# Optimization experiments

Measured on AMD Instinct MI355X. Metric: run time of the kernel, lower is better.

The kernel has to match this reference:

```python
import jax, jax.numpy as jnp
import numpy as np

H = 512
W = 512
N_STROKES = 5000
S = 10          # samples_per_curve
K = 20          # strokes_per_pixel
CANVAS_COLOR = 0.5  # 'gray'
COARSE = 5      # coarse grid downsample factor (H//5, W//5)


def setup_inputs() -> dict:
    key = jax.random.key(0)
    ks = jax.random.split(key, 6)
    # stroke centers spread over the canvas
    location = jax.random.uniform(ks[0], (N_STROKES, 2), jnp.float32) * jnp.array([H, W], jnp.float32)
    # bezier control-point offsets relative to the stroke center
    curve_s = jax.random.normal(ks[1], (N_STROKES, 2), jnp.float32) * 8.0
    curve_e = jax.random.normal(ks[2], (N_STROKES, 2), jnp.float32) * 8.0
    curve_c = jax.random.normal(ks[3], (N_STROKES, 2), jnp.float32) * 8.0
    color = jax.random.uniform(ks[4], (N_STROKES, 3), jnp.float32)
    width = jax.random.uniform(ks[5], (N_STROKES, 1), jnp.float32) * 4.0 + 1.0
    return {"curve_s": curve_s, "curve_e": curve_e, "curve_c": curve_c,
            "color": color, "location": location, "width": width}


def _bezier_points(s, c, e, num_points):
    # s, c, e: [N, 2] -> [N, num_points, 2]
    t = jnp.linspace(0.0, 1.0, num_points).astype(jnp.float32)  # [S]
    omt2 = (1.0 - t) ** 2  # [S]
    t2 = t ** 2
    # x/y computed identically: c + (1-t)^2 (s - c) + t^2 (e - c)
    pts = c[:, None, :] + omt2[None, :, None] * (s - c)[:, None, :] \
          + t2[None, :, None] * (e - c)[:, None, :]
    return pts  # [N, S, 2]


def _nearest_upsample_idx(out_size, in_size):
    # torch F.interpolate mode='nearest': src = floor(dst * in/out)
    idx = jnp.floor(jnp.arange(out_size) * (in_size / out_size)).astype(jnp.int32)
    return jnp.clip(idx, 0, in_size - 1)


def reference(curve_s, curve_e, curve_c, color, location, width):
    # sample bezier curve points (absolute coords)
    pts = _bezier_points(curve_s + location, curve_c + location,
                         curve_e + location, S)  # [N, S, 2]

    # ---- coarse-grid KNN over stroke centers ----
    Hc, Wc = H // COARSE, W // COARSE
    tH = jnp.linspace(0.0, float(H), Hc).astype(jnp.float32)
    tW = jnp.linspace(0.0, float(W), Wc).astype(jnp.float32)
    Px, Py = jnp.meshgrid(tH, tW, indexing='ij')
    P = jnp.stack([Px, Py], axis=-1)  # [Hc, Wc, 2]
    D_centers = jnp.sum(jnp.square(P[:, :, None, :] - location), axis=-1)  # [Hc, Wc, N]
    _, idcs = jax.lax.top_k(-D_centers, K)  # [Hc, Wc, K]

    near_pts = pts[idcs]      # [Hc, Wc, K, S, 2]
    near_col = color[idcs]    # [Hc, Wc, K, 3]
    near_w = width[idcs]      # [Hc, Wc, K, 1]

    # ---- upsample coarse gathers to full res ----
    ih = _nearest_upsample_idx(H, Hc)
    iw = _nearest_upsample_idx(W, Wc)
    near_pts = near_pts[ih][:, iw]   # [H, W, K, S, 2] (nearest)
    near_col = near_col[ih][:, iw]   # [H, W, K, 3]   (nearest)
    # widths: bilinear (align_corners=False, no antialias) per channel
    near_w = jax.image.resize(near_w[..., 0], (H, W, K), method='linear')[..., None]  # [H, W, K, 1]

    # ---- full-res pixel grid ----
    tHf = jnp.linspace(0.0, float(H), H).astype(jnp.float32)
    tWf = jnp.linspace(0.0, float(W), W).astype(jnp.float32)
    Pxf, Pyf = jnp.meshgrid(tHf, tWf, indexing='ij')
    P_full = jnp.stack([Pxf, Pyf], axis=-1)  # [H, W, 2]

    # ---- per-pixel closest point on each polyline segment ----
    a = near_pts[:, :, :, :S - 1, :]              # [H, W, K, S-1, 2]
    b_a = near_pts[:, :, :, 1:, :] - a            # segment direction
    pa = P_full[:, :, None, None, :] - a          # pixel - segment start
    t = jnp.sum(b_a * pa, axis=-1) / jnp.sum(jnp.square(b_a), axis=-1)
    t = jnp.clip(t, 0.0, 1.0)
    closest = a + t[..., None] * b_a
    dist = jnp.sum(jnp.square(P_full[:, :, None, None, :] - closest), axis=-1)  # [H, W, K, S-1]

    D = jnp.min(dist, axis=(-1, -2))  # [H, W]
    min_per_stroke = jnp.min(dist, axis=-1)  # [H, W, K]
    ranking = jax.nn.softmax(100000.0 * (1.0 / (1e-08 + min_per_stroke)), axis=-1)  # [H, W, K]

    I_colors = jnp.einsum('hwkf,hwk->hwf', near_col, ranking)  # [H, W, 3]
    bs = jnp.einsum('hwkf,hwk->hwf', near_w, ranking)          # [H, W, 1]
    bs_mask = jax.nn.sigmoid(bs - D[..., None])
    canvas = jnp.full_like(I_colors, CANVAS_COLOR)
    I = I_colors * bs_mask + (1.0 - bs_mask) * canvas
    return I
```

## Files before the change

kernel.cpp:

```cpp
#include <hip/hip_runtime.h>
#include <math.h>

#define NS 5000
#define SS 10
#define KK 20
#define HC 102
#define NBIN 32
#define BINW 16.0f
#define NPB 20
#define CAP 192

#define WAVE_SYNC() __asm__ volatile("s_waitcnt lgkmcnt(0)" ::: "memory")

__global__ void __launch_bounds__(256) prep_kernel(
        const float* __restrict__ cs, const float* __restrict__ ce,
        const float* __restrict__ cc, const float* __restrict__ loc,
        const float* __restrict__ color, const float* __restrict__ width,
        float* __restrict__ sdata, float4* __restrict__ ctab,
        int* __restrict__ binCntP) {
    __shared__ int4 lcnt4[NBIN*NBIN/4];
    int* lcnt = (int*)lcnt4;
    int t = threadIdx.x;
    lcnt4[t] = make_int4(0, 0, 0, 0);
    __syncthreads();
    int i = blockIdx.x * 256 + t;
    if (i < NS) {
        float lx = loc[i*2+0], ly = loc[i*2+1];
        float sx = cs[i*2+0] + lx, sy = cs[i*2+1] + ly;
        float ex = ce[i*2+0] + lx, ey = ce[i*2+1] + ly;
        float px = cc[i*2+0] + lx, py = cc[i*2+1] + ly;
        float qx[SS], qy[SS];
        #pragma unroll
        for (int j = 0; j < SS; ++j) {
            float tt = (float)j * (1.0f / 9.0f);
            float omt = 1.0f - tt;
            float omt2 = omt * omt, t2 = tt * tt;
            qx[j] = px + omt2 * (sx - px) + t2 * (ex - px);
            qy[j] = py + omt2 * (sy - py) + t2 * (ey - py);
            sdata[i*32 + 2*j + 0] = qx[j];
            sdata[i*32 + 2*j + 1] = qy[j];
        }
        #pragma unroll
        for (int sg = 0; sg < 9; ++sg) {
            float bx = qx[sg+1] - qx[sg], by = qy[sg+1] - qy[sg];
            sdata[i*32 + 20 + sg] = 1.0f / (bx*bx + by*by);
        }
        sdata[i*32 + 29] = 0.0f; sdata[i*32 + 30] = 0.0f; sdata[i*32 + 31] = 0.0f;
        ctab[i] = make_float4(color[i*3+0], color[i*3+1], color[i*3+2], width[i]);
        int b0 = min(max((int)(lx * (1.0f/BINW)), 0), NBIN-1);
        int b1 = min(max((int)(ly * (1.0f/BINW)), 0), NBIN-1);
        atomicAdd(&lcnt[b0*NBIN + b1], 1);
    }
    __syncthreads();
    ((int4*)binCntP)[blockIdx.x * 256 + t] = lcnt4[t];
}

__global__ void __launch_bounds__(256) scatter_kernel(
        const float* __restrict__ loc, const int* __restrict__ binCntP,
        int* __restrict__ binStart, float2* __restrict__ sxy, int* __restrict__ sid) {
    __shared__ int fill[NBIN*NBIN];
    __shared__ int wsum[4];
    int t = threadIdx.x, lane = t & 63, w = t >> 6;
    int mb = blockIdx.x;
    int4 tot = make_int4(0,0,0,0), bel = make_int4(0,0,0,0);
    for (int b = 0; b < NPB; ++b) {
        int4 v = ((const int4*)binCntP)[b * 256 + t];
        tot.x += v.x; tot.y += v.y; tot.z += v.z; tot.w += v.w;
        if (b < mb) { bel.x += v.x; bel.y += v.y; bel.z += v.z; bel.w += v.w; }
    }
    int s0 = tot.x, s1 = s0 + tot.y, s2 = s1 + tot.z, s3 = s2 + tot.w;
    int x = s3;
    #pragma unroll
    for (int off = 1; off < 64; off <<= 1) {
        int y = __shfl_up(x, off, 64);
        if (lane >= off) x += y;
    }
    if (lane == 63) wsum[w] = x;
    __syncthreads();
    int woff = 0;
    #pragma unroll
    for (int i = 0; i < 4; ++i) woff += (i < w) ? wsum[i] : 0;
    int texcl = woff + x - s3;
    fill[4*t+0] = texcl      + bel.x;
    fill[4*t+1] = texcl + s0 + bel.y;
    fill[4*t+2] = texcl + s1 + bel.z;
    fill[4*t+3] = texcl + s2 + bel.w;
    if (mb == 0) {
        binStart[4*t+1] = texcl + s0;
        binStart[4*t+2] = texcl + s1;
        binStart[4*t+3] = texcl + s2;
        binStart[4*t+4] = texcl + s3;
        if (t == 0) binStart[0] = 0;
    }
    __syncthreads();
    int i = mb * 256 + t;
    if (i < NS) {
        float l0 = loc[i*2+0], l1 = loc[i*2+1];
        int b0 = min(max((int)(l0 * (1.0f/BINW)), 0), NBIN-1);
        int b1 = min(max((int)(l1 * (1.0f/BINW)), 0), NBIN-1);
        int pos = atomicAdd(&fill[b0*NBIN + b1], 1);
        sxy[pos] = make_float2(l0, l1);
        sid[pos] = i;
    }
}

__global__ void __launch_bounds__(256) topk_kernel(const float* __restrict__ loc,
                                                   const float* __restrict__ width,
                                                   const float2* __restrict__ sxy,
                                                   const int* __restrict__ sid,
                                                   const int* __restrict__ binStart,
                                                   int* __restrict__ idcs,
                                                   float* __restrict__ wk) {
    __shared__ unsigned long long sk[4][CAP];
    int w = threadIdx.x >> 6, lane = threadIdx.x & 63;
    int cell = blockIdx.x * 4 + w;
    int ci = cell / HC, cj = cell - ci * HC;
    const float dc = 512.0f / 101.0f;
    float c0 = (float)ci * dc;
    float c1 = (float)cj * dc;
    unsigned long long below = (1ull << lane) - 1ull;

    float R = 26.0f;
    int cnt = 0;
    for (int attempt = 0; attempt < 5; ++attempt) {
        float R2 = R * R;
        int base = 0;
        int by0 = max((int)((c0 - R) * (1.0f/BINW)), 0);
        int by1 = min((int)((c0 + R) * (1.0f/BINW)), NBIN-1);
        int bx0 = max((int)((c1 - R) * (1.0f/BINW)), 0);
        int bx1 = min((int)((c1 + R) * (1.0f/BINW)), NBIN-1);
        int nrows = by1 - by0 + 1;
        if (nrows <= 6) {
            int rs[6], re[6];
            #pragma unroll
            for (int r = 0; r < 6; ++r) {
                bool va = (r < nrows);
                int by = va ? (by0 + r) : by0;
                rs[r] = binStart[by*NBIN + bx0];
                re[r] = va ? binStart[by*NBIN + bx1 + 1] : rs[r];
            }
            float2 pr[6]; int idr[6];
            #pragma unroll
            for (int r = 0; r < 6; ++r) {
                int t  = rs[r] + lane;
                int tc = max(min(t, re[r] - 1), 0);
                pr[r]  = sxy[tc];
                idr[r] = sid[tc];
            }
            #pragma unroll
            for (int r = 0; r < 6; ++r) {
                int t = rs[r] + lane;
                float dx = c0 - pr[r].x, dy = c1 - pr[r].y;
                float d = dx*dx + dy*dy;
                bool pred = (t < re[r]) && (d < R2);
                unsigned long long mask = __ballot(pred);
                int pos = base + __popcll(mask & below);
                if (pred && pos < CAP)
                    sk[w][pos] = ((unsigned long long)__float_as_uint(d) << 32)
                               | (unsigned int)idr[r];
                base += __popcll(mask);
                for (int t0 = rs[r] + 64; t0 < re[r]; t0 += 64) {
                    int t2  = t0 + lane;
                    int tc2 = min(t2, re[r] - 1);
                    float2 p = sxy[tc2];
                    float ex = c0 - p.x, ey = c1 - p.y;
                    float d2 = ex*ex + ey*ey;
                    bool p2 = (t2 < re[r]) && (d2 < R2);
                    unsigned long long m2 = __ballot(p2);
                    int pos2 = base + __popcll(m2 & below);
                    if (p2 && pos2 < CAP)
                        sk[w][pos2] = ((unsigned long long)__float_as_uint(d2) << 32)
                                    | (unsigned int)sid[tc2];
                    base += __popcll(m2);
                }
            }
        } else {
            for (int by = by0; by <= by1; ++by) {
                int s = binStart[by*NBIN + bx0];
                int e = binStart[by*NBIN + bx1 + 1];
                for (int t0 = s; t0 < e; t0 += 64) {
                    int t = t0 + lane;
                    int tc = min(t, e - 1);
                    float2 p = sxy[tc];
                    float dx = c0 - p.x, dy = c1 - p.y;
                    float d = dx*dx + dy*dy;
                    bool pred = (t < e) && (d < R2);
                    unsigned long long mask = __ballot(pred);
                    int pos = base + __popcll(mask & below);
                    if (pred && pos < CAP)
                        sk[w][pos] = ((unsigned long long)__float_as_uint(d) << 32)
                                   | (unsigned int)sid[tc];
                    base += __popcll(mask);
                }
            }
        }
        cnt = base;
        if (cnt >= KK) break;
        R *= 1.6f;
    }
    WAVE_SYNC();

    if (cnt >= KK && cnt <= CAP) {
        if (cnt <= 64) {
            unsigned long long k0 = (lane < cnt) ? sk[w][lane] : ~0ull;
            int r0 = 0;
            int j = 0;
            #pragma unroll 1
            for (; j + 4 <= cnt; j += 4) {
                unsigned long long a = sk[w][j],   b = sk[w][j+1];
                unsigned long long c = sk[w][j+2], d = sk[w][j+3];
                r0 += (int)(a < k0) + (int)(b < k0) + (int)(c < k0) + (int)(d < k0);
            }
            for (; j < cnt; ++j) r0 += (int)(sk[w][j] < k0);
            if (r0 < KK && lane < cnt) {
                int idx = (int)(unsigned int)(k0 & 0xffffffffull);
                idcs[cell*KK + r0] = idx;
                wk[cell*KK + r0]   = width[idx];
            }
        } else {
            unsigned long long k0 = (lane       < cnt) ? sk[w][lane]       : ~0ull;
            unsigned long long k1 = (lane + 64  < cnt) ? sk[w][lane + 64]  : ~0ull;
            unsigned long long k2 = (lane + 128 < cnt) ? sk[w][lane + 128] : ~0ull;
            int r0 = 0, r1 = 0, r2 = 0;
            #pragma unroll 1
            for (int j = 0; j < cnt; ++j) {
                unsigned long long a = sk[w][j];
                r0 += (int)(a < k0); r1 += (int)(a < k1); r2 += (int)(a < k2);
            }
            if (r0 < KK && lane < cnt) {
                int idx = (int)(unsigned int)(k0 & 0xffffffffull);
                idcs[cell*KK + r0] = idx;  wk[cell*KK + r0] = width[idx];
            }
            if (r1 < KK && lane + 64 < cnt) {
                int idx = (int)(unsigned int)(k1 & 0xffffffffull);
                idcs[cell*KK + r1] = idx;  wk[cell*KK + r1] = width[idx];
            }
            if (r2 < KK && lane + 128 < cnt) {
                int idx = (int)(unsigned int)(k2 & 0xffffffffull);
                idcs[cell*KK + r2] = idx;  wk[cell*KK + r2] = width[idx];
            }
        }
    } else {
        if (lane == 0) {
            float bd[KK]; int bi[KK];
            for (int k = 0; k < KK; ++k) { bd[k] = 3.4e38f; bi[k] = 0; }
            for (int n = 0; n < NS; ++n) {
                float dx = c0 - loc[n*2+0];
                float dy = c1 - loc[n*2+1];
                float d = dx*dx + dy*dy;
                if (d < bd[KK-1]) {
                    int p = KK - 1;
                    while (p > 0 && bd[p-1] > d) { bd[p] = bd[p-1]; bi[p] = bi[p-1]; --p; }
                    bd[p] = d; bi[p] = n;
                }
            }
            for (int k = 0; k < KK; ++k) {
                idcs[cell*KK + k] = bi[k];
                wk[cell*KK + k]   = width[bi[k]];
            }
        }
    }
}

__global__ void __launch_bounds__(256, 4) render_kernel(const float* __restrict__ sdata,
                                                        const float4* __restrict__ ctab,
                                                        const int* __restrict__ idcs,
                                                        const float* __restrict__ wk,
                                                        float* __restrict__ out) {
    __shared__ float wvl[256][21];
    int tt0 = threadIdx.x, lane = tt0 & 63, wq = tt0 >> 6;
    int x = blockIdx.x * 16 + ((wq & 1) << 3) + (lane & 7);
    int y = blockIdx.y * 16 + ((wq >> 1) << 3) + (lane >> 3);
    const float df = 512.0f / 511.0f;
    float p0 = (float)y * df;
    float p1 = (float)x * df;
    int cy = (y * 51) >> 8;
    int cx = (x * 51) >> 8;

    const int4* mip = (const int4*)(idcs + (cy * HC + cx) * KK);
    int4 m0 = mip[0], m1 = mip[1], m2 = mip[2], m3 = mip[3], m4 = mip[4];
    int idxs[KK] = {m0.x,m0.y,m0.z,m0.w, m1.x,m1.y,m1.z,m1.w, m2.x,m2.y,m2.z,m2.w,
                    m3.x,m3.y,m3.z,m3.w, m4.x,m4.y,m4.z,m4.w};

    const float sc = 102.0f / 512.0f;
    float iny = ((float)y + 0.5f) * sc - 0.5f;
    float inx = ((float)x + 0.5f) * sc - 0.5f;
    float y0f = floorf(iny), x0f = floorf(inx);
    float fy = iny - y0f, fx = inx - x0f;
    int y0 = min(max((int)y0f, 0), HC - 1);
    int y1 = min(max((int)y0f + 1, 0), HC - 1);
    int x0 = min(max((int)x0f, 0), HC - 1);
    int x1 = min(max((int)x0f + 1, 0), HC - 1);
    const float4* q00 = (const float4*)(wk + (y0 * HC + x0) * KK);
    const float4* q01 = (const float4*)(wk + (y0 * HC + x1) * KK);
    const float4* q10 = (const float4*)(wk + (y1 * HC + x0) * KK);
    const float4* q11 = (const float4*)(wk + (y1 * HC + x1) * KK);

    #pragma unroll
    for (int r = 0; r < 5; ++r) {
        float4 a = q00[r], b = q01[r], c = q10[r], d = q11[r];
        wvl[tt0][4*r+0] = (1.0f - fy) * ((1.0f - fx) * a.x + fx * b.x)
                        +          fy * ((1.0f - fx) * c.x + fx * d.x);
        wvl[tt0][4*r+1] = (1.0f - fy) * ((1.0f - fx) * a.y + fx * b.y)
                        +          fy * ((1.0f - fx) * c.y + fx * d.y);
        wvl[tt0][4*r+2] = (1.0f - fy) * ((1.0f - fx) * a.z + fx * b.z)
                        +          fy * ((1.0f - fx) * c.z + fx * d.z);
        wvl[tt0][4*r+3] = (1.0f - fy) * ((1.0f - fx) * a.w + fx * b.w)
                        +          fy * ((1.0f - fx) * c.w + fx * d.w);
    }

    float m = -INFINITY, s = 0.0f;
    float a0 = 0.0f, a1 = 0.0f, a2 = 0.0f, wa = 0.0f;
    float D = INFINITY;

    #pragma unroll 4
    for (int k = 0; k < KK; ++k) {
        const float4* sp = (const float4*)(sdata + idxs[k] * 32);
        float4 f0 = sp[0], f1 = sp[1], f2 = sp[2], f3 = sp[3], f4 = sp[4];
        float4 i0 = sp[5], i1 = sp[6], i2 = sp[7];
        float4 cw = ctab[idxs[k]];
        float qx[10] = {f0.x, f0.z, f1.x, f1.z, f2.x, f2.z, f3.x, f3.z, f4.x, f4.z};
        float qy[10] = {f0.y, f0.w, f1.y, f1.w, f2.y, f2.w, f3.y, f3.w, f4.y, f4.w};
        float iv[9]  = {i0.x, i0.y, i0.z, i0.w, i1.x, i1.y, i1.z, i1.w, i2.x};
        float mink = INFINITY;
        #pragma unroll
        for (int sg = 0; sg < 9; ++sg) {
            float ax = qx[sg], ay = qy[sg];
            float bx = qx[sg+1] - ax, by = qy[sg+1] - ay;
            float pax = p0 - ax, pay = p1 - ay;
            float dot = bx * pax + by * pay;
            float tt = dot * iv[sg];
            tt = fminf(fmaxf(tt, 0.0f), 1.0f);
            float ccx = ax + tt * bx, ccy = ay + tt * by;
            float ddx = p0 - ccx, ddy = p1 - ccy;
            float d = ddx * ddx + ddy * ddy;
            mink = fminf(mink, d);
        }
        D = fminf(D, mink);
        float z = 100000.0f / (1e-8f + mink);
        float nm  = fmaxf(m, z);
        float scl = __expf(m - nm);
        float e   = __expf(z - nm);
        s  = s  * scl + e;
        a0 = a0 * scl + cw.x * e;
        a1 = a1 * scl + cw.y * e;
        a2 = a2 * scl + cw.z * e;
        wa = wa * scl + wvl[tt0][k] * e;
        m = nm;
    }
    float inv = 1.0f / s;
    float bs = wa * inv;
    float msk = 1.0f / (1.0f + __expf(-(bs - D)));
    float o0 = a0 * inv * msk + (1.0f - msk) * 0.5f;
    float o1 = a1 * inv * msk + (1.0f - msk) * 0.5f;
    float o2 = a2 * inv * msk + (1.0f - msk) * 0.5f;
    int base = (y * 512 + x) * 3;
    out[base+0] = o0;
    out[base+1] = o1;
    out[base+2] = o2;
}

extern "C" void kernel_launch(void* const* d_in, const int* in_sizes, int n_in,
                              void* d_out, int out_size, void* d_ws, size_t ws_size,
                              hipStream_t stream) {
    const float* cs    = (const float*)d_in[0];
    const float* ce    = (const float*)d_in[1];
    const float* cc    = (const float*)d_in[2];
    const float* color = (const float*)d_in[3];
    const float* loc   = (const float*)d_in[4];
    const float* width = (const float*)d_in[5];
    float* out = (float*)d_out;

    char* p = (char*)d_ws;
    float*  sdata    = (float*)p;                 p += NS * 32 * sizeof(float);
    float4* ctab     = (float4*)p;                p += NS * sizeof(float4);
    int*    idcs     = (int*)p;                   p += (size_t)HC*HC*KK*sizeof(int);
    float*  wk       = (float*)p;                 p += (size_t)HC*HC*KK*sizeof(float);
    int*    binCntP  = (int*)p;                   p += NPB * NBIN*NBIN * sizeof(int);
    int*    binStart = (int*)p;                   p += 4112;
    float2* sxy      = (float2*)p;                p += NS * sizeof(float2);
    int*    sid      = (int*)p;

    prep_kernel   <<<NPB, 256, 0, stream>>>(cs, ce, cc, loc, color, width, sdata, ctab, binCntP);
    scatter_kernel<<<NPB, 256, 0, stream>>>(loc, binCntP, binStart, sxy, sid);
    topk_kernel   <<<(HC*HC)/4, 256, 0, stream>>>(loc, width, sxy, sid, binStart, idcs, wk);
    render_kernel <<<dim3(32, 32), 256, 0, stream>>>(sdata, ctab, idcs, wk, out);
}
```

Measured before the change: 128.3 us.

## Stage per-block stroke records and colors in LDS for render kernel

The render kernel now loads, for each 16x16 pixel block, the up to 16 coarse cells it covers. It copies their 20 stroke indices, 32-float stroke records and color entries into shared memory once per block. The inner loop then reads them from LDS rather than gathering from global memory per pixel. The bilinear width interpolation moves into the loop and reads global wk directly instead of going through a per-thread LDS array. This cuts redundant scattered global loads but uses about 47 KB of LDS per block, which may lower occupancy below the launch-bounds target, and it adds a staging phase with two barriers.

```diff
diff --git a/kernel.cpp b/kernel.cpp
--- a/kernel.cpp
+++ b/kernel.cpp
@@ -267,20 +267,34 @@
                                                         const int* __restrict__ idcs,
                                                         const float* __restrict__ wk,
                                                         float* __restrict__ out) {
-    __shared__ float wvl[256][21];
+    __shared__ float  srec[16*20*32];
+    __shared__ float4 scol[16*20];
+    __shared__ int    sidx[16*20];
     int tt0 = threadIdx.x, lane = tt0 & 63, wq = tt0 >> 6;
     int x = blockIdx.x * 16 + ((wq & 1) << 3) + (lane & 7);
     int y = blockIdx.y * 16 + ((wq >> 1) << 3) + (lane >> 3);
+    int cy0 = (blockIdx.y * 16 * 51) >> 8;
+    int cx0 = (blockIdx.x * 16 * 51) >> 8;
+
+    for (int s = tt0; s < 16*20; s += 256) {
+        int c = s / 20, k = s - c * 20;
+        int cellI = (cy0 + (c >> 2)) * HC + cx0 + (c & 3);
+        sidx[s] = idcs[cellI * KK + k];
+    }
+    __syncthreads();
+    for (int s = tt0; s < 16*20*8; s += 256) {
+        int r = s >> 3, wd = s & 7;
+        ((float4*)srec)[s] = ((const float4*)sdata)[sidx[r] * 8 + wd];
+    }
+    for (int s = tt0; s < 16*20; s += 256) scol[s] = ctab[sidx[s]];
+    __syncthreads();
+
     const float df = 512.0f / 511.0f;
     float p0 = (float)y * df;
     float p1 = (float)x * df;
     int cy = (y * 51) >> 8;
     int cx = (x * 51) >> 8;
-
-    const int4* mip = (const int4*)(idcs + (cy * HC + cx) * KK);
-    int4 m0 = mip[0], m1 = mip[1], m2 = mip[2], m3 = mip[3], m4 = mip[4];
-    int idxs[KK] = {m0.x,m0.y,m0.z,m0.w, m1.x,m1.y,m1.z,m1.w, m2.x,m2.y,m2.z,m2.w,
-                    m3.x,m3.y,m3.z,m3.w, m4.x,m4.y,m4.z,m4.w};
+    int lc = ((cy - cy0) << 2) + (cx - cx0);
 
     const float sc = 102.0f / 512.0f;
     float iny = ((float)y + 0.5f) * sc - 0.5f;
@@ -291,23 +305,10 @@
     int y1 = min(max((int)y0f + 1, 0), HC - 1);
     int x0 = min(max((int)x0f, 0), HC - 1);
     int x1 = min(max((int)x0f + 1, 0), HC - 1);
-    const float4* q00 = (const float4*)(wk + (y0 * HC + x0) * KK);
-    const float4* q01 = (const float4*)(wk + (y0 * HC + x1) * KK);
-    const float4* q10 = (const float4*)(wk + (y1 * HC + x0) * KK);
-    const float4* q11 = (const float4*)(wk + (y1 * HC + x1) * KK);
-
-    #pragma unroll
-    for (int r = 0; r < 5; ++r) {
-        float4 a = q00[r], b = q01[r], c = q10[r], d = q11[r];
-        wvl[tt0][4*r+0] = (1.0f - fy) * ((1.0f - fx) * a.x + fx * b.x)
-                        +          fy * ((1.0f - fx) * c.x + fx * d.x);
-        wvl[tt0][4*r+1] = (1.0f - fy) * ((1.0f - fx) * a.y + fx * b.y)
-                        +          fy * ((1.0f - fx) * c.y + fx * d.y);
-        wvl[tt0][4*r+2] = (1.0f - fy) * ((1.0f - fx) * a.z + fx * b.z)
-                        +          fy * ((1.0f - fx) * c.z + fx * d.z);
-        wvl[tt0][4*r+3] = (1.0f - fy) * ((1.0f - fx) * a.w + fx * b.w)
-                        +          fy * ((1.0f - fx) * c.w + fx * d.w);
-    }
+    const float* w00 = wk + (y0 * HC + x0) * KK;
+    const float* w01 = wk + (y0 * HC + x1) * KK;
+    const float* w10 = wk + (y1 * HC + x0) * KK;
+    const float* w11 = wk + (y1 * HC + x1) * KK;
 
     float m = -INFINITY, s = 0.0f;
     float a0 = 0.0f, a1 = 0.0f, a2 = 0.0f, wa = 0.0f;
@@ -315,10 +316,10 @@
 
     #pragma unroll 4
     for (int k = 0; k < KK; ++k) {
-        const float4* sp = (const float4*)(sdata + idxs[k] * 32);
+        const float4* sp = (const float4*)(srec + (lc * 20 + k) * 32);
         float4 f0 = sp[0], f1 = sp[1], f2 = sp[2], f3 = sp[3], f4 = sp[4];
         float4 i0 = sp[5], i1 = sp[6], i2 = sp[7];
-        float4 cw = ctab[idxs[k]];
+        float4 cw = scol[lc * 20 + k];
         float qx[10] = {f0.x, f0.z, f1.x, f1.z, f2.x, f2.z, f3.x, f3.z, f4.x, f4.z};
         float qy[10] = {f0.y, f0.w, f1.y, f1.w, f2.y, f2.w, f3.y, f3.w, f4.y, f4.w};
         float iv[9]  = {i0.x, i0.y, i0.z, i0.w, i1.x, i1.y, i1.z, i1.w, i2.x};
@@ -338,6 +339,8 @@
         }
         D = fminf(D, mink);
         float z = 100000.0f / (1e-8f + mink);
+        float wkv = (1.0f - fy) * ((1.0f - fx) * w00[k] + fx * w01[k])
+                  +          fy * ((1.0f - fx) * w10[k] + fx * w11[k]);
         float nm  = fmaxf(m, z);
         float scl = __expf(m - nm);
         float e   = __expf(z - nm);
@@ -345,7 +348,7 @@
         a0 = a0 * scl + cw.x * e;
         a1 = a1 * scl + cw.y * e;
         a2 = a2 * scl + cw.z * e;
-        wa = wa * scl + wvl[tt0][k] * e;
+        wa = wa * scl + wkv * e;
         m = nm;
     }
     float inv = 1.0f / s;
```

New measurement: 116.9 us. 8.9% less time.
